# Optimization experiments

Measured on AMD Instinct MI355X. Metric: run time of the kernel, lower is better.

The kernel has to match this reference:

```python
import jax, jax.numpy as jnp
import numpy as np

B, S, H, NH = 1, 4096, 1024, 16
HD = H // NH  # head_dim = 64
ROPE_BASE = 10000.0


def setup_inputs() -> dict:
    key = jax.random.key(0)
    ks = jax.random.split(key, 8)
    sc = 0.02
    return {
        "hidden_states": jax.random.normal(ks[0], (B, S, H), jnp.float32),
        "attention_mask": jnp.zeros((B, 1, 1, S), jnp.float32),
        "Wq": jax.random.normal(ks[1], (H, H), jnp.float32) * sc,
        "bq": jnp.zeros((H,), jnp.float32),
        "Wk": jax.random.normal(ks[2], (H, H), jnp.float32) * sc,
        "bk": jnp.zeros((H,), jnp.float32),
        "Wv": jax.random.normal(ks[3], (H, H), jnp.float32) * sc,
        "bv": jnp.zeros((H,), jnp.float32),
    }


def _rope_tables(seq_len, head_dim, dtype):
    inv_freq = 1.0 / (ROPE_BASE ** (jnp.arange(0, head_dim, 2, dtype=jnp.float32) / head_dim))
    t = jnp.arange(seq_len, dtype=jnp.float32)
    freqs = jnp.einsum("s,d->sd", t, inv_freq)          # [S, HD/2]
    emb = jnp.concatenate([freqs, freqs], axis=-1)       # [S, HD]
    return jnp.cos(emb).astype(dtype), jnp.sin(emb).astype(dtype)


def _rotate_half(x):
    x1, x2 = jnp.split(x, 2, axis=-1)
    return jnp.concatenate([-x2, x1], axis=-1)


def reference(hidden_states, attention_mask, Wq, bq, Wk, bk, Wv, bv):
    bsz, q_len, _ = hidden_states.shape
    # QKV projections (torch Linear: x @ W.T + b), split into heads -> [B, NH, S, HD]
    def heads(x):
        return x.reshape(bsz, q_len, NH, HD).transpose(0, 2, 1, 3)
    q = heads(hidden_states @ Wq.T + bq)
    k = heads(hidden_states @ Wk.T + bk)
    v = heads(hidden_states @ Wv.T + bv)

    # RoPE with position_ids = arange(kv_seq_len)
    cos, sin = _rope_tables(q_len, HD, q.dtype)          # [S, HD]
    cos = cos[None, None]                                 # [1,1,S,HD]
    sin = sin[None, None]
    q = q * cos + _rotate_half(q) * sin
    k = k * cos + _rotate_half(k) * sin

    # Manual scaled-dot-product attention (baddbmm + softmax + matmul)
    scale = HD ** (-0.5)
    scores = jnp.einsum("bhqd,bhkd->bhqk", q, k) * scale  # [B,NH,S,S]
    scores = scores + attention_mask                      # broadcast additive mask
    weights = jax.nn.softmax(scores, axis=-1)
    attn = jnp.einsum("bhqk,bhkd->bhqd", weights, v)      # [B,NH,S,HD]

    # [B,S,NH,HD] -> [B,S,H]
    return attn.transpose(0, 2, 1, 3).reshape(bsz, q_len, NH * HD)
```

## Files before the change

kernel.cpp:

```cpp
#include <hip/hip_runtime.h>
#include <hip/hip_bf16.h>
#include <math.h>
#include <stdint.h>

#define S_ 4096
#define H_ 1024
#define NH_ 16
#define HD_ 64
#define LOG2E 1.4426950408889634f
#define QSCALE (0.125f * LOG2E)

typedef __bf16 bf16;
typedef __attribute__((ext_vector_type(8))) __bf16 bf16x8;
typedef __attribute__((ext_vector_type(4))) __bf16 bf16x4;
typedef __attribute__((ext_vector_type(4))) float f32x4;
typedef __attribute__((ext_vector_type(16))) float f32x16;
typedef __attribute__((ext_vector_type(2))) float f32x2;
typedef __attribute__((ext_vector_type(2))) int int2v;

__device__ __forceinline__ f32x4 mfma16(bf16x8 a, bf16x8 b, f32x4 c) {
    return __builtin_amdgcn_mfma_f32_16x16x32_bf16(a, b, c, 0, 0, 0);
}
__device__ __forceinline__ f32x16 mfma32(bf16x8 a, bf16x8 b, f32x16 c) {
    return __builtin_amdgcn_mfma_f32_32x32x16_bf16(a, b, c, 0, 0, 0);
}

__device__ __forceinline__ void gload16(const void* g, void* l) {
    __builtin_amdgcn_global_load_lds(
        (__attribute__((address_space(1))) void*)(uintptr_t)g,
        (__attribute__((address_space(3))) void*)(uintptr_t)l,
        16, 0, 0);
}

__device__ __forceinline__ unsigned cvtpk(float a, float b) {
    unsigned r;
    asm("v_cvt_pk_bf16_f32 %0, %1, %2" : "=v"(r) : "v"(a), "v"(b));
    return r;
}

__device__ __forceinline__ void swap32(unsigned a, unsigned b, unsigned& r0, unsigned& r1) {
#if __has_builtin(__builtin_amdgcn_permlane32_swap)
    int2v rr = __builtin_amdgcn_permlane32_swap((int)a, (int)b, false, false);
    r0 = (unsigned)rr[0];
    r1 = (unsigned)rr[1];
#else
    unsigned sa = (unsigned)__shfl_xor((int)a, 32, 64);
    unsigned sb = (unsigned)__shfl_xor((int)b, 32, 64);
    bool hi = (threadIdx.x & 32) != 0;
    r0 = hi ? sb : a;
    r1 = hi ? b : sa;
#endif
}

__device__ __forceinline__ float fexp2(float x) {
#if __has_builtin(__builtin_amdgcn_exp2f)
    return __builtin_amdgcn_exp2f(x);
#else
    return exp2f(x);
#endif
}

__global__ __launch_bounds__(256) void cvt_all_kernel(
    const float* __restrict__ hs, const float* __restrict__ Wq,
    const float* __restrict__ Wk, const float* __restrict__ Wv,
    bf16* __restrict__ Xb, bf16* __restrict__ Wqb,
    bf16* __restrict__ Wkb, bf16* __restrict__ Wvb) {
    int b = blockIdx.x;
    const float* src; bf16* dst; size_t base;
    if (b < 2048)      { src = hs; dst = Xb;  base = (size_t)b * 2048; }
    else if (b < 2560) { src = Wq; dst = Wqb; base = (size_t)(b - 2048) * 2048; }
    else if (b < 3072) { src = Wk; dst = Wkb; base = (size_t)(b - 2560) * 2048; }
    else               { src = Wv; dst = Wvb; base = (size_t)(b - 3072) * 2048; }
    size_t i = base + threadIdx.x * 8;
    float4 v0 = *reinterpret_cast<const float4*>(src + i);
    float4 v1 = *reinterpret_cast<const float4*>(src + i + 4);
    bf16x8 o;
    o[0] = (bf16)v0.x; o[1] = (bf16)v0.y; o[2] = (bf16)v0.z; o[3] = (bf16)v0.w;
    o[4] = (bf16)v1.x; o[5] = (bf16)v1.y; o[6] = (bf16)v1.z; o[7] = (bf16)v1.w;
    *reinterpret_cast<bf16x8*>(dst + i) = o;
}

__global__ __launch_bounds__(256) void prep_kernel(const float* __restrict__ mask,
                                                   float2* __restrict__ tab,
                                                   bf16* __restrict__ wM,
                                                   float* __restrict__ wV) {
    int idx = blockIdx.x * 256 + threadIdx.x;
    if (idx < S_ * 32) {
        int i = idx & 31, s = idx >> 5;
        double ang = (double)s * exp(-(double)(2 * i) / 64.0 * log(10000.0));
        tab[idx] = make_float2((float)cos(ang), (float)sin(ang));
    }
    if (idx < S_) {
        float e = exp2f(mask[idx] * LOG2E);
        bf16 eb = (bf16)e;
        wM[idx] = eb;
        wV[idx] = (float)eb;
    }
}

__global__ __launch_bounds__(256) void qkv_gemm_kernel(
    const bf16* __restrict__ Xb,
    const bf16* __restrict__ Wqb, const bf16* __restrict__ Wkb, const bf16* __restrict__ Wvb,
    const float* __restrict__ bqp, const float* __restrict__ bkp, const float* __restrict__ bvp,
    const float2* __restrict__ tab, const float* __restrict__ wV,
    bf16* __restrict__ Qo, bf16* __restrict__ Ko, bf16* __restrict__ Vto)
{
    __shared__ bf16 Alds[128 * 64];
    __shared__ bf16 Blds[128 * 64];
    const int z = blockIdx.z;
    const bf16* W = z == 0 ? Wqb : z == 1 ? Wkb : Wvb;
    const float* bias = z == 0 ? bqp : z == 1 ? bkp : bvp;
    const int tm = blockIdx.y * 128, tn = blockIdx.x * 128;
    const int tid = threadIdx.x, lane = tid & 63, wid = tid >> 6;
    const int wm = (wid >> 1) * 64, wn = (wid & 1) * 64;
    const int lr = lane & 15, lg = lane >> 4;
    const int c_row = tid >> 3, c_sub = tid & 7;

    f32x4 acc[4][4] = {};

    for (int kt = 0; kt < H_; kt += 64) {
        #pragma unroll
        for (int is = 0; is < 4; ++is) {
            int row = is * 32 + c_row;
            int sub = c_sub ^ (row & 7);
            gload16(&Xb[(size_t)(tm + row) * H_ + kt + sub * 8],
                    &Alds[(is * 256 + wid * 64) * 8]);
            gload16(&W[(size_t)(tn + row) * H_ + kt + sub * 8],
                    &Blds[(is * 256 + wid * 64) * 8]);
        }
        __syncthreads();

        #pragma unroll
        for (int kc = 0; kc < 2; ++kc) {
            bf16x8 af[4], bfr[4];
            #pragma unroll
            for (int mb = 0; mb < 4; ++mb) {
                int row = wm + mb * 16 + lr;
                int ch = (kc * 4 + lg) ^ (row & 7);
                af[mb] = *reinterpret_cast<const bf16x8*>(&Alds[row * 64 + ch * 8]);
            }
            #pragma unroll
            for (int nb = 0; nb < 4; ++nb) {
                int row = wn + nb * 16 + lr;
                int ch = (kc * 4 + lg) ^ (row & 7);
                bfr[nb] = *reinterpret_cast<const bf16x8*>(&Blds[row * 64 + ch * 8]);
            }
            #pragma unroll
            for (int mb = 0; mb < 4; ++mb)
                #pragma unroll
                for (int nb = 0; nb < 4; ++nb)
                    acc[mb][nb] = mfma16(af[mb], bfr[nb], acc[mb][nb]);
        }
        __syncthreads();
    }

    float bv4[4];
    #pragma unroll
    for (int nb = 0; nb < 4; ++nb) bv4[nb] = bias[tn + wn + nb * 16 + lr];

    if (z < 2) {
        bf16* Y = z == 0 ? Qo : Ko;
        const float fs = z == 0 ? QSCALE : 1.0f;
        #pragma unroll
        for (int mb = 0; mb < 4; ++mb) {
            #pragma unroll
            for (int r = 0; r < 4; ++r) {
                int row = tm + wm + mb * 16 + lg * 4 + r;
                #pragma unroll
                for (int nb = 0; nb < 2; ++nb) {
                    float2 cs = tab[row * 32 + nb * 16 + lr];
                    float x1 = acc[mb][nb][r] + bv4[nb];
                    float x2 = acc[mb][nb + 2][r] + bv4[nb + 2];
                    int col = tn + wn + nb * 16 + lr;
                    Y[(size_t)row * H_ + col]      = (bf16)((x1 * cs.x - x2 * cs.y) * fs);
                    Y[(size_t)row * H_ + col + 32] = (bf16)((x2 * cs.x + x1 * cs.y) * fs);
                }
            }
        }
    } else {
        #pragma unroll
        for (int mb = 0; mb < 4; ++mb) {
            int rowb = tm + wm + mb * 16 + lg * 4;
            float4 wv = *reinterpret_cast<const float4*>(&wV[rowb]);
            float wvr[4] = {wv.x, wv.y, wv.z, wv.w};
            #pragma unroll
            for (int nb = 0; nb < 4; ++nb) {
                int col = tn + wn + nb * 16 + lr;
                bf16x4 pk;
                #pragma unroll
                for (int r = 0; r < 4; ++r)
                    pk[r] = (bf16)((acc[mb][nb][r] + bv4[nb]) * wvr[r]);
                *reinterpret_cast<bf16x4*>(&Vto[(size_t)col * S_ + rowb]) = pk;
            }
        }
    }
}

__global__ __launch_bounds__(256) void attn_kernel(
    const bf16* __restrict__ Q, const bf16* __restrict__ K, const bf16* __restrict__ Vt,
    const bf16* __restrict__ wM, float* __restrict__ out)
{
    __shared__ bf16 Kl[2][64 * 64];
    __shared__ bf16 Vl[3][64 * 64];
    const int h = blockIdx.y;
    const int qb = blockIdx.x * 128;
    const int tid = threadIdx.x, lane = tid & 63, wid = tid >> 6;
    const int l31 = lane & 31, hi = lane >> 5;
    const int srow = wid * 8 + (lane >> 3);
    const int ssub = (lane & 7) ^ (srow & 7);

    bf16x8 qf[4];
    {
        const bf16* qp = &Q[(size_t)(qb + wid * 32 + l31) * H_ + h * 64 + hi * 8];
        #pragma unroll
        for (int ks = 0; ks < 4; ++ks)
            qf[ks] = *reinterpret_cast<const bf16x8*>(qp + ks * 16);
    }

    f32x16 o0 = {}, o1 = {}, lacc = {};

    const bf16* kg = &K[(size_t)srow * H_ + h * 64 + ssub * 8];
    const bf16* vg = &Vt[(size_t)(h * 64 + srow) * S_ + ssub * 8];

    auto STAGE_K = [&](int buf) {
        gload16(kg,           &Kl[buf][(wid * 8) * 64]);
        gload16(kg + 32 * H_, &Kl[buf][(32 + wid * 8) * 64]);
        kg += 64 * H_;
    };
    auto STAGE_V = [&](int buf) {
        gload16(vg,           &Vl[buf][(wid * 8) * 64]);
        gload16(vg + 32 * S_, &Vl[buf][(32 + wid * 8) * 64]);
        vg += 64;
    };

    auto QK = [&](const bf16* Kb_, f32x16& q0, f32x16& q1) {
        f32x16 a = {}, b = {};
        __builtin_amdgcn_s_setprio(1);
        #pragma unroll
        for (int ks = 0; ks < 4; ++ks) {
            int ch = (2 * ks + hi) ^ (l31 & 7);
            bf16x8 kf0 = *reinterpret_cast<const bf16x8*>(&Kb_[l31 * 64 + ch * 8]);
            a = mfma32(kf0, qf[ks], a);
            bf16x8 kf1 = *reinterpret_cast<const bf16x8*>(&Kb_[(32 + l31) * 64 + ch * 8]);
            b = mfma32(kf1, qf[ks], b);
        }
        __builtin_amdgcn_s_setprio(0);
        q0 = a; q1 = b;
    };

    STAGE_K(0); STAGE_V(0);
    STAGE_K(1); STAGE_V(1);
    __syncthreads();

    f32x16 scA0, scA1, scB0, scB1;
    QK(Kl[0], scA0, scA1);

    int vstage = 2;
    int vread = 0;
    const bf16* wmt = wM + hi * 8;
    const int NT = S_ / 64;

    auto BODY = [&](int t, f32x16& sm0, f32x16& sm1, f32x16& qk0, f32x16& qk1) {
        __syncthreads();
        if (t + 1 < NT) QK(Kl[(t + 1) & 1], qk0, qk1);
        if (t + 2 < NT) {
            STAGE_K(t & 1);
            STAGE_V(vstage);
            vstage = vstage == 2 ? 0 : vstage + 1;
        }

        #pragma unroll
        for (int r = 0; r < 16; ++r) sm0[r] = fexp2(sm0[r]);
        #pragma unroll
        for (int r = 0; r < 16; ++r) sm1[r] = fexp2(sm1[r]);

        bf16x8 pf[4];
        #pragma unroll
        for (int ks = 0; ks < 2; ++ks) {
            unsigned w[4];
            #pragma unroll
            for (int wi = 0; wi < 2; ++wi) {
                unsigned u = cvtpk(sm0[8 * ks + 2 * wi],     sm0[8 * ks + 2 * wi + 1]);
                unsigned v = cvtpk(sm0[8 * ks + 4 + 2 * wi], sm0[8 * ks + 4 + 2 * wi + 1]);
                swap32(u, v, w[wi], w[wi + 2]);
            }
            union { unsigned u[4]; bf16x8 v; } cv;
            cv.u[0] = w[0]; cv.u[1] = w[1]; cv.u[2] = w[2]; cv.u[3] = w[3];
            pf[ks] = cv.v;
        }
        #pragma unroll
        for (int ks = 0; ks < 2; ++ks) {
            unsigned w[4];
            #pragma unroll
            for (int wi = 0; wi < 2; ++wi) {
                unsigned u = cvtpk(sm1[8 * ks + 2 * wi],     sm1[8 * ks + 2 * wi + 1]);
                unsigned v = cvtpk(sm1[8 * ks + 4 + 2 * wi], sm1[8 * ks + 4 + 2 * wi + 1]);
                swap32(u, v, w[wi], w[wi + 2]);
            }
            union { unsigned u[4]; bf16x8 v; } cv;
            cv.u[0] = w[0]; cv.u[1] = w[1]; cv.u[2] = w[2]; cv.u[3] = w[3];
            pf[2 + ks] = cv.v;
        }

        const bf16* Vb_ = Vl[vread];
        __builtin_amdgcn_s_setprio(1);
        #pragma unroll
        for (int ks = 0; ks < 4; ++ks) {
            int ch = (2 * ks + hi) ^ (l31 & 7);
            bf16x8 vf0 = *reinterpret_cast<const bf16x8*>(&Vb_[l31 * 64 + ch * 8]);
            o0 = mfma32(vf0, pf[ks], o0);
            bf16x8 vf1 = *reinterpret_cast<const bf16x8*>(&Vb_[(32 + l31) * 64 + ch * 8]);
            o1 = mfma32(vf1, pf[ks], o1);
            bf16x8 wf = *reinterpret_cast<const bf16x8*>(wmt + ks * 16);
            lacc = mfma32(wf, pf[ks], lacc);
        }
        __builtin_amdgcn_s_setprio(0);
        wmt += 64;
        vread = vread == 2 ? 0 : vread + 1;
    };

    for (int t = 0; t < NT; t += 2) {
        BODY(t,     scA0, scA1, scB0, scB1);
        BODY(t + 1, scB0, scB1, scA0, scA1);
    }

    float inv = 1.f / lacc[0];
    float* orow = &out[(size_t)(qb + wid * 32 + l31) * H_ + h * 64];
    #pragma unroll
    for (int g2 = 0; g2 < 4; ++g2) {
        float4 a, b;
        a.x = o0[g2 * 4 + 0] * inv; a.y = o0[g2 * 4 + 1] * inv;
        a.z = o0[g2 * 4 + 2] * inv; a.w = o0[g2 * 4 + 3] * inv;
        b.x = o1[g2 * 4 + 0] * inv; b.y = o1[g2 * 4 + 1] * inv;
        b.z = o1[g2 * 4 + 2] * inv; b.w = o1[g2 * 4 + 3] * inv;
        *reinterpret_cast<float4*>(orow + 8 * g2 + 4 * hi) = a;
        *reinterpret_cast<float4*>(orow + 32 + 8 * g2 + 4 * hi) = b;
    }
}

extern "C" void kernel_launch(void* const* d_in, const int* in_sizes, int n_in,
                              void* d_out, int out_size, void* d_ws, size_t ws_size,
                              hipStream_t stream) {
    const float* hs   = (const float*)d_in[0];
    const float* mask = (const float*)d_in[1];
    const float* Wq   = (const float*)d_in[2];
    const float* bq   = (const float*)d_in[3];
    const float* Wk   = (const float*)d_in[4];
    const float* bk   = (const float*)d_in[5];
    const float* Wv   = (const float*)d_in[6];
    const float* bv   = (const float*)d_in[7];
    float* out = (float*)d_out;

    char* ws = (char*)d_ws;
    bf16* Xb    = (bf16*)(ws);
    bf16* Wqb   = (bf16*)(ws + (8u  << 20));
    bf16* Wkb   = (bf16*)(ws + (10u << 20));
    bf16* Wvb   = (bf16*)(ws + (12u << 20));
    bf16* Qb    = (bf16*)(ws + (14u << 20));
    bf16* Kb    = (bf16*)(ws + (22u << 20));
    bf16* Vt    = (bf16*)(ws + (30u << 20));
    float2* tab = (float2*)(ws + (38u << 20));
    bf16* wM    = (bf16*)(ws + (39u << 20));
    float* wV   = (float*)(ws + (39u << 20) + 65536);

    cvt_all_kernel<<<3584, 256, 0, stream>>>(hs, Wq, Wk, Wv, Xb, Wqb, Wkb, Wvb);
    prep_kernel<<<(S_ * 32) / 256, 256, 0, stream>>>(mask, tab, wM, wV);
    qkv_gemm_kernel<<<dim3(H_ / 128, S_ / 128, 3), 256, 0, stream>>>(
        Xb, Wqb, Wkb, Wvb, bq, bk, bv, tab, wV, Qb, Kb, Vt);
    attn_kernel<<<dim3(S_ / 128, NH_), 256, 0, stream>>>(Qb, Kb, Vt, wM, out);
}
```

Before: 152.9 us.

## Deepen attention K/V pipeline to four stages and fuse prep into cvt kernel

The attention kernel now uses four-slot K and V LDS rings and prefetches three tiles ahead. It replaces __syncthreads with explicit vmcnt waits and raw barriers, so each iteration waits only for the oldest outstanding loads. Separately, the RoPE table and mask-weight prep kernel is folded into the conversion kernel, which removes one launch. LDS use grows from 40KB to 64KB per block, which may lower occupancy, and the hand-counted vmcnt(4) must match the number of in-flight loads.

```diff
diff --git a/kernel.cpp b/kernel.cpp
--- a/kernel.cpp
+++ b/kernel.cpp
@@ -63,8 +63,10 @@
 __global__ __launch_bounds__(256) void cvt_all_kernel(
     const float* __restrict__ hs, const float* __restrict__ Wq,
     const float* __restrict__ Wk, const float* __restrict__ Wv,
+    const float* __restrict__ mask,
     bf16* __restrict__ Xb, bf16* __restrict__ Wqb,
-    bf16* __restrict__ Wkb, bf16* __restrict__ Wvb) {
+    bf16* __restrict__ Wkb, bf16* __restrict__ Wvb,
+    float2* __restrict__ tab, bf16* __restrict__ wM, float* __restrict__ wV) {
     int b = blockIdx.x;
     const float* src; bf16* dst; size_t base;
     if (b < 2048)      { src = hs; dst = Xb;  base = (size_t)b * 2048; }
@@ -78,16 +80,11 @@
     o[0] = (bf16)v0.x; o[1] = (bf16)v0.y; o[2] = (bf16)v0.z; o[3] = (bf16)v0.w;
     o[4] = (bf16)v1.x; o[5] = (bf16)v1.y; o[6] = (bf16)v1.z; o[7] = (bf16)v1.w;
     *reinterpret_cast<bf16x8*>(dst + i) = o;
-}
-
-__global__ __launch_bounds__(256) void prep_kernel(const float* __restrict__ mask,
-                                                   float2* __restrict__ tab,
-                                                   bf16* __restrict__ wM,
-                                                   float* __restrict__ wV) {
-    int idx = blockIdx.x * 256 + threadIdx.x;
+
+    int idx = b * 256 + threadIdx.x;
     if (idx < S_ * 32) {
-        int i = idx & 31, s = idx >> 5;
-        double ang = (double)s * exp(-(double)(2 * i) / 64.0 * log(10000.0));
+        int ii = idx & 31, s = idx >> 5;
+        double ang = (double)s * exp(-(double)(2 * ii) / 64.0 * log(10000.0));
         tab[idx] = make_float2((float)cos(ang), (float)sin(ang));
     }
     if (idx < S_) {
@@ -200,8 +197,8 @@
     const bf16* __restrict__ Q, const bf16* __restrict__ K, const bf16* __restrict__ Vt,
     const bf16* __restrict__ wM, float* __restrict__ out)
 {
-    __shared__ bf16 Kl[2][64 * 64];
-    __shared__ bf16 Vl[3][64 * 64];
+    __shared__ bf16 Kl[4][64 * 64];
+    __shared__ bf16 Vl[4][64 * 64];
     const int h = blockIdx.y;
     const int qb = blockIdx.x * 128;
     const int tid = threadIdx.x, lane = tid & 63, wid = tid >> 6;
@@ -222,14 +219,13 @@
     const bf16* kg = &K[(size_t)srow * H_ + h * 64 + ssub * 8];
     const bf16* vg = &Vt[(size_t)(h * 64 + srow) * S_ + ssub * 8];
 
-    auto STAGE_K = [&](int buf) {
+    auto STAGE = [&](int tile) {
+        const int buf = tile & 3;
         gload16(kg,           &Kl[buf][(wid * 8) * 64]);
         gload16(kg + 32 * H_, &Kl[buf][(32 + wid * 8) * 64]);
-        kg += 64 * H_;
-    };
-    auto STAGE_V = [&](int buf) {
         gload16(vg,           &Vl[buf][(wid * 8) * 64]);
         gload16(vg + 32 * S_, &Vl[buf][(32 + wid * 8) * 64]);
+        kg += 64 * H_;
         vg += 64;
     };
 
@@ -248,26 +244,27 @@
         q0 = a; q1 = b;
     };
 
-    STAGE_K(0); STAGE_V(0);
-    STAGE_K(1); STAGE_V(1);
-    __syncthreads();
+    const int NT = S_ / 64;
+
+    STAGE(0); STAGE(1); STAGE(2);
+    asm volatile("s_waitcnt vmcnt(0)" ::: "memory");
+    __builtin_amdgcn_s_barrier();
+    __builtin_amdgcn_sched_barrier(0);
 
     f32x16 scA0, scA1, scB0, scB1;
     QK(Kl[0], scA0, scA1);
 
-    int vstage = 2;
-    int vread = 0;
     const bf16* wmt = wM + hi * 8;
-    const int NT = S_ / 64;
 
     auto BODY = [&](int t, f32x16& sm0, f32x16& sm1, f32x16& qk0, f32x16& qk1) {
-        __syncthreads();
-        if (t + 1 < NT) QK(Kl[(t + 1) & 1], qk0, qk1);
-        if (t + 2 < NT) {
-            STAGE_K(t & 1);
-            STAGE_V(vstage);
-            vstage = vstage == 2 ? 0 : vstage + 1;
-        }
+        __builtin_amdgcn_sched_barrier(0);
+        if (t >= NT - 2) asm volatile("s_waitcnt vmcnt(0)" ::: "memory");
+        else             asm volatile("s_waitcnt vmcnt(4)" ::: "memory");
+        __builtin_amdgcn_s_barrier();
+        __builtin_amdgcn_sched_barrier(0);
+
+        if (t + 1 < NT) QK(Kl[(t + 1) & 3], qk0, qk1);
+        if (t + 3 < NT) STAGE(t + 3);
 
         #pragma unroll
         for (int r = 0; r < 16; ++r) sm0[r] = fexp2(sm0[r]);
@@ -302,7 +299,7 @@
             pf[2 + ks] = cv.v;
         }
 
-        const bf16* Vb_ = Vl[vread];
+        const bf16* Vb_ = Vl[t & 3];
         __builtin_amdgcn_s_setprio(1);
         #pragma unroll
         for (int ks = 0; ks < 4; ++ks) {
@@ -316,7 +313,6 @@
         }
         __builtin_amdgcn_s_setprio(0);
         wmt += 64;
-        vread = vread == 2 ? 0 : vread + 1;
     };
 
     for (int t = 0; t < NT; t += 2) {
@@ -363,8 +359,8 @@
     bf16* wM    = (bf16*)(ws + (39u << 20));
     float* wV   = (float*)(ws + (39u << 20) + 65536);
 
-    cvt_all_kernel<<<3584, 256, 0, stream>>>(hs, Wq, Wk, Wv, Xb, Wqb, Wkb, Wvb);
-    prep_kernel<<<(S_ * 32) / 256, 256, 0, stream>>>(mask, tab, wM, wV);
+    cvt_all_kernel<<<3584, 256, 0, stream>>>(hs, Wq, Wk, Wv, mask,
+                                             Xb, Wqb, Wkb, Wvb, tab, wM, wV);
     qkv_gemm_kernel<<<dim3(H_ / 128, S_ / 128, 3), 256, 0, stream>>>(
         Xb, Wqb, Wkb, Wvb, bq, bk, bv, tab, wV, Qb, Kb, Vt);
     attn_kernel<<<dim3(S_ / 128, NH_), 256, 0, stream>>>(Qb, Kb, Vt, wM, out);
```

After: 153.1 us. Within noise of the previous version (+0.2%).
